# Kernel tuning notes

Measured on AMD Instinct MI355X. Metric: run time of the kernel, lower is better.

Reference implementation:

```python
import jax, jax.numpy as jnp
import numpy as np

B, S, D, H, L, O = 64, 512, 512, 1024, 2, 1000


def setup_inputs() -> dict:
    key = jax.random.key(0)
    ks = jax.random.split(key, 12)
    s = 0.05
    return {
        "x": jax.random.normal(ks[0], (B, S, D), jnp.float32),
        "h0": jnp.zeros((L, B, H), jnp.float32),
        "c0": jnp.zeros((L, B, H), jnp.float32),
        "W_ih0": jax.random.normal(ks[1], (4 * H, D), jnp.float32) * s,
        "W_hh0": jax.random.normal(ks[2], (4 * H, H), jnp.float32) * s,
        "b_ih0": jax.random.normal(ks[3], (4 * H,), jnp.float32) * s,
        "b_hh0": jax.random.normal(ks[4], (4 * H,), jnp.float32) * s,
        "W_ih1": jax.random.normal(ks[5], (4 * H, H), jnp.float32) * s,
        "W_hh1": jax.random.normal(ks[6], (4 * H, H), jnp.float32) * s,
        "b_ih1": jax.random.normal(ks[7], (4 * H,), jnp.float32) * s,
        "b_hh1": jax.random.normal(ks[8], (4 * H,), jnp.float32) * s,
        "W_fc": jax.random.normal(ks[9], (O, H), jnp.float32) * s,
        "b_fc": jax.random.normal(ks[10], (O,), jnp.float32) * s,
    }


def _lstm_cell(x_t, h, c, W_ih, W_hh, b_ih, b_hh):
    # standard LSTMCell: fused 4-gate GEMM, gate order (i, f, g, o)
    gates = x_t @ W_ih.T + b_ih + h @ W_hh.T + b_hh  # [B, 4H]
    i, f, g, o = jnp.split(gates, 4, axis=-1)
    i = jax.nn.sigmoid(i)
    f = jax.nn.sigmoid(f)
    g = jnp.tanh(g)
    o = jax.nn.sigmoid(o)
    c_new = f * c + i * g
    h_new = o * jnp.tanh(c_new)
    return h_new, c_new


def reference(x, h0, c0, W_ih0, W_hh0, b_ih0, b_hh0, W_ih1, W_hh1, b_ih1, b_hh1, W_fc, b_fc):
    params = [(W_ih0, W_hh0, b_ih0, b_hh0), (W_ih1, W_hh1, b_ih1, b_hh1)]

    def step(carry, x_t):
        hs, cs = carry  # tuples of [B,H] per layer
        new_h, new_c = [], []
        inp = x_t
        for l in range(L):  # fixed small layer count
            h_l, c_l = _lstm_cell(inp, hs[l], cs[l], *params[l])
            new_h.append(h_l)
            new_c.append(c_l)
            inp = h_l
        return (tuple(new_h), tuple(new_c)), None

    xs = jnp.swapaxes(x, 0, 1)  # [S, B, D]
    init = (tuple(h0[l] for l in range(L)), tuple(c0[l] for l in range(L)))
    (hs, _), _ = jax.lax.scan(step, init, xs)
    # dropout is inference-mode identity; output_activation=None
    out = hs[-1] @ W_fc.T + b_fc  # [B, O]
    return out
```

## Files before the change

### kernel.cpp

```cpp
#include <hip/hip_runtime.h>

#define B_ 64
#define S_ 512
#define D_ 512
#define H_ 1024

typedef __attribute__((ext_vector_type(8))) short bf16x8;
typedef __attribute__((ext_vector_type(4))) float f32x4;
typedef unsigned short u16;
typedef unsigned int u32;

#define MFMA(a, b, c) __builtin_amdgcn_mfma_f32_16x16x32_bf16(a, b, c, 0, 0, 0)

__device__ __forceinline__ u16 f2bf(float f) {
    u32 u = __float_as_uint(f);
    u += 0x7fffu + ((u >> 16) & 1u);
    return (u16)(u >> 16);
}
__device__ __forceinline__ float sigm(float x) { return 1.0f / (1.0f + __expf(-x)); }
__device__ __forceinline__ float tanh_f(float x) { return 1.0f - 2.0f / (__expf(2.0f * x) + 1.0f); }

__device__ __forceinline__ bf16x8 cvt8(const float* p) {
    float4 f0 = ((const float4*)p)[0];
    float4 f1 = ((const float4*)p)[1];
    bf16x8 v;
    v[0] = (short)f2bf(f0.x); v[1] = (short)f2bf(f0.y);
    v[2] = (short)f2bf(f0.z); v[3] = (short)f2bf(f0.w);
    v[4] = (short)f2bf(f1.x); v[5] = (short)f2bf(f1.y);
    v[6] = (short)f2bf(f1.z); v[7] = (short)f2bf(f1.w);
    return v;
}

__device__ __forceinline__ void llc_ld(bf16x8& d, const u16* p) {
    asm volatile("global_load_dwordx4 %0, %1, off sc0 sc1" : "=v"(d) : "v"(p));
}
__device__ __forceinline__ void vm0() {
    asm volatile("s_waitcnt vmcnt(0)" ::: "memory");
}
__device__ __forceinline__ void fence_frag(bf16x8& d) {
    asm volatile("" : "+v"(d));
}
__device__ __forceinline__ void llc_st16(u16* p, u16 v) {
    u32 vv = v;
    asm volatile("global_store_short %0, %1, off sc0 sc1" :: "v"(p), "v"(vv) : "memory");
}

__global__ void prep_w(const float* __restrict__ Wih, const float* __restrict__ Whh,
                       u16* __restrict__ Wc, int Kx, int Kw, int total8) {
    int idx = blockIdx.x * 256 + threadIdx.x;
    if (idx >= total8) return;
    int kc8 = Kw >> 3;
    int n = idx / kc8;
    int kc = (idx - n * kc8) << 3;
    const float* src = (kc < Kx) ? (Wih + (size_t)n * Kx + kc)
                                 : (Whh + (size_t)n * (Kw - Kx) + (kc - Kx));
    *(bf16x8*)(Wc + (size_t)n * Kw + kc) = cvt8(src);
}

__global__ void prep_misc2(const float* __restrict__ h0in,
                           const float* __restrict__ bih0, const float* __restrict__ bhh0,
                           const float* __restrict__ bih1, const float* __restrict__ bhh1,
                           float* __restrict__ bias0, float* __restrict__ bias1,
                           u16* __restrict__ h0a, u16* __restrict__ h0b,
                           u16* __restrict__ h1a, u16* __restrict__ h1b,
                           int* __restrict__ bar) {
    int idx = blockIdx.x * 256 + threadIdx.x;
    if (idx < 1024) bar[idx] = 0;
    if (idx < 4096) { bias0[idx] = bih0[idx] + bhh0[idx]; return; }
    if (idx < 8192) { int i = idx - 4096; bias1[i] = bih1[i] + bhh1[i]; return; }
    int r = idx - 8192;
    if (r >= 2 * B_ * H_) return;
    int l = r >> 16;
    int rr = r & 65535;
    int b = rr >> 10, col = rr & 1023;
    int sidx = (col >> 3) * 512 + b * 8 + (col & 7);
    u16 hb = f2bf(h0in[r]);
    if (l == 0) { h0a[sidx] = hb; h0b[sidx] = hb; }
    else        { h1a[sidx] = hb; h1b[sidx] = hb; }
}

__global__ __launch_bounds__(512, 2) void lstm_persist(
    const float* __restrict__ x,
    const u16* __restrict__ W0c, const u16* __restrict__ W1c,
    const float* __restrict__ bias0, const float* __restrict__ bias1,
    const float* __restrict__ c0in,
    u16* __restrict__ h0a, u16* __restrict__ h0b,
    u16* __restrict__ h1a, u16* __restrict__ h1b,
    float* __restrict__ h1f,
    int* __restrict__ bar) {
    const int bk = blockIdx.x;
    const int cgp = bk >> 1;
    const int mh = bk & 1;
    const int tid = threadIdx.x;
    const int w = tid >> 6;
    const int lane = tid & 63;
    const int quad = lane >> 4;
    const int l16 = lane & 15;

    int gc[2];
    #pragma unroll
    for (int n = 0; n < 2; ++n) {
        int c = n * 16 + l16;
        gc[n] = (c >> 3) * 1024 + cgp * 8 + (c & 7);
    }

    bf16x8 w0x[2][2], w0h[2][4];
    bf16x8 w1f[2][8];
    #pragma unroll
    for (int n = 0; n < 2; ++n) {
        #pragma unroll
        for (int kf = 0; kf < 2; ++kf)
            w0x[n][kf] = *(const bf16x8*)(W0c + (size_t)gc[n] * 1536 + w * 64 + kf * 32 + quad * 8);
        #pragma unroll
        for (int kf = 0; kf < 4; ++kf)
            w0h[n][kf] = *(const bf16x8*)(W0c + (size_t)gc[n] * 1536 + 512 + w * 128 + kf * 32 + quad * 8);
        #pragma unroll
        for (int kf = 0; kf < 8; ++kf)
            w1f[n][kf] = *(const bf16x8*)(W1c + (size_t)gc[n] * 2048 + w * 256 + kf * 32 + quad * 8);
    }

    __shared__ float part[8 * 32 * 37];
    __shared__ float c0l[256], c1l[256];
    __shared__ float b0l[32], b1l[32];

    if (tid < 32) {
        int gg = tid >> 3, j = tid & 7;
        b0l[tid] = bias0[gg * 1024 + cgp * 8 + j];
        b1l[tid] = bias1[gg * 1024 + cgp * 8 + j];
    }
    if (tid < 256) {
        int b = tid >> 3, j = tid & 7;
        int gi = (mh * 32 + b) * 1024 + cgp * 8 + j;
        c0l[tid] = c0in[gi];
        c1l[tid] = c0in[65536 + gi];
    }
    __syncthreads();

    const int brow0 = mh * 32 + l16;
    const int brow1 = brow0 + 16;

    f32x4 xacc[2][2];
    #define XPART(t)                                                                 \
        {                                                                            \
            xacc[0][0] = (f32x4){0.f,0.f,0.f,0.f}; xacc[0][1] = (f32x4){0.f,0.f,0.f,0.f}; \
            xacc[1][0] = (f32x4){0.f,0.f,0.f,0.f}; xacc[1][1] = (f32x4){0.f,0.f,0.f,0.f}; \
            _Pragma("unroll")                                                        \
            for (int kf = 0; kf < 2; ++kf) {                                         \
                int k = w * 64 + kf * 32 + quad * 8;                                 \
                bf16x8 a0_ = cvt8(x + (size_t)brow0 * 262144 + (t) * 512 + k);       \
                bf16x8 a1_ = cvt8(x + (size_t)brow1 * 262144 + (t) * 512 + k);       \
                xacc[0][0] = MFMA(a0_, w0x[0][kf], xacc[0][0]);                      \
                xacc[0][1] = MFMA(a0_, w0x[1][kf], xacc[0][1]);                      \
                xacc[1][0] = MFMA(a1_, w0x[0][kf], xacc[1][0]);                      \
                xacc[1][1] = MFMA(a1_, w0x[1][kf], xacc[1][1]);                      \
            }                                                                        \
        }

    XPART(0);

    for (int p = 0; p <= S_; ++p) {
        const int rd = p & 1;
        const u16* h0r = rd ? h0b : h0a;
        u16*       h0w_ = rd ? h0a : h0b;
        const u16* h1r = rd ? h1b : h1a;
        u16*       h1w_ = rd ? h1a : h1b;

        if (p > 0) {
            if (tid == 0) {
                int target = 256 * p;
                for (int it = 0; it < 20000; ++it) {
                    if (__hip_atomic_load(&bar[0], __ATOMIC_RELAXED, __HIP_MEMORY_SCOPE_AGENT) >= target)
                        break;
                    __builtin_amdgcn_s_sleep(1);
                }
            }
            __syncthreads();
        }

        bf16x8 a0[4], a1[4];
        if (p < S_) {
            #pragma unroll
            for (int kf = 0; kf < 4; ++kf) {
                int k8 = w * 16 + kf * 4 + quad;
                llc_ld(a0[kf], h0r + (k8 * 64 + brow0) * 8);
                llc_ld(a1[kf], h0r + (k8 * 64 + brow1) * 8);
            }
            vm0();
            #pragma unroll
            for (int kf = 0; kf < 4; ++kf) { fence_frag(a0[kf]); fence_frag(a1[kf]); }
        }
        bf16x8 pb0[8], pb1[8];
        if (p >= 1) {
            #pragma unroll
            for (int kf = 0; kf < 8; ++kf) {
                int k = w * 256 + kf * 32;
                const u16* src = (k < 1024) ? h0r : h1r;
                int k8 = ((k & 1023) >> 3) + quad;
                llc_ld(pb0[kf], src + (k8 * 64 + brow0) * 8);
                llc_ld(pb1[kf], src + (k8 * 64 + brow1) * 8);
            }
        }

        if (p < S_) {
            f32x4 acc00 = xacc[0][0], acc01 = xacc[0][1];
            f32x4 acc10 = xacc[1][0], acc11 = xacc[1][1];
            #pragma unroll
            for (int kf = 0; kf < 4; ++kf) {
                acc00 = MFMA(a0[kf], w0h[0][kf], acc00);
                acc01 = MFMA(a0[kf], w0h[1][kf], acc01);
                acc10 = MFMA(a1[kf], w0h[0][kf], acc10);
                acc11 = MFMA(a1[kf], w0h[1][kf], acc11);
            }
            #pragma unroll
            for (int r = 0; r < 4; ++r) {
                int r0 = quad * 4 + r, r1 = 16 + quad * 4 + r;
                part[w * 1184 + r0 * 37 + l16]      = acc00[r];
                part[w * 1184 + r0 * 37 + 16 + l16] = acc01[r];
                part[w * 1184 + r1 * 37 + l16]      = acc10[r];
                part[w * 1184 + r1 * 37 + 16 + l16] = acc11[r];
            }
            __syncthreads();
            if (tid < 256) {
                int b = tid >> 3, j = tid & 7;
                float g4[4];
                #pragma unroll
                for (int gg = 0; gg < 4; ++gg) {
                    float s = b0l[gg * 8 + j];
                    #pragma unroll
                    for (int w8 = 0; w8 < 8; ++w8)
                        s += part[w8 * 1184 + b * 37 + gg * 8 + j];
                    g4[gg] = s;
                }
                float c = c0l[tid];
                float cn = sigm(g4[1]) * c + sigm(g4[0]) * tanh_f(g4[2]);
                float hn = sigm(g4[3]) * tanh_f(cn);
                c0l[tid] = cn;
                llc_st16(h0w_ + cgp * 512 + (mh * 32 + b) * 8 + j, f2bf(hn));
            }
            __syncthreads();
        }

        if (p >= 1) {
            vm0();
            #pragma unroll
            for (int kf = 0; kf < 8; ++kf) { fence_frag(pb0[kf]); fence_frag(pb1[kf]); }
            f32x4 acc00 = {0.f,0.f,0.f,0.f}, acc01 = {0.f,0.f,0.f,0.f};
            f32x4 acc10 = {0.f,0.f,0.f,0.f}, acc11 = {0.f,0.f,0.f,0.f};
            #pragma unroll
            for (int kf = 0; kf < 8; ++kf) {
                acc00 = MFMA(pb0[kf], w1f[0][kf], acc00);
                acc01 = MFMA(pb0[kf], w1f[1][kf], acc01);
                acc10 = MFMA(pb1[kf], w1f[0][kf], acc10);
                acc11 = MFMA(pb1[kf], w1f[1][kf], acc11);
            }
            #pragma unroll
            for (int r = 0; r < 4; ++r) {
                int r0 = quad * 4 + r, r1 = 16 + quad * 4 + r;
                part[w * 1184 + r0 * 37 + l16]      = acc00[r];
                part[w * 1184 + r0 * 37 + 16 + l16] = acc01[r];
                part[w * 1184 + r1 * 37 + l16]      = acc10[r];
                part[w * 1184 + r1 * 37 + 16 + l16] = acc11[r];
            }
            __syncthreads();
            if (tid < 256) {
                int b = tid >> 3, j = tid & 7;
                float g4[4];
                #pragma unroll
                for (int gg = 0; gg < 4; ++gg) {
                    float s = b1l[gg * 8 + j];
                    #pragma unroll
                    for (int w8 = 0; w8 < 8; ++w8)
                        s += part[w8 * 1184 + b * 37 + gg * 8 + j];
                    g4[gg] = s;
                }
                float c = c1l[tid];
                float cn = sigm(g4[1]) * c + sigm(g4[0]) * tanh_f(g4[2]);
                float hn = sigm(g4[3]) * tanh_f(cn);
                c1l[tid] = cn;
                llc_st16(h1w_ + cgp * 512 + (mh * 32 + b) * 8 + j, f2bf(hn));
                if (p == S_) h1f[(mh * 32 + b) * 1024 + cgp * 8 + j] = hn;
            }
            __syncthreads();
        }

        if (p < S_) {
            if (tid == 0)
                __hip_atomic_fetch_add(&bar[0], 1, __ATOMIC_RELAXED, __HIP_MEMORY_SCOPE_AGENT);
            if (p + 1 < S_) XPART(p + 1);
        }
    }
}

__global__ void fc_k(const float* __restrict__ h1f, const float* __restrict__ Wfc,
                     const float* __restrict__ bfc, float* __restrict__ out) {
    int idx = blockIdx.x * 256 + threadIdx.x;
    if (idx >= 64 * 1000) return;
    int o = idx % 1000;
    int b = idx / 1000;
    const float4* hr = (const float4*)(h1f + b * H_);
    const float4* wr = (const float4*)(Wfc + (size_t)o * H_);
    float s = 0.f;
    #pragma unroll 4
    for (int k = 0; k < 256; ++k) {
        float4 a = hr[k];
        float4 w = wr[k];
        s += a.x * w.x + a.y * w.y + a.z * w.z + a.w * w.w;
    }
    out[idx] = s + bfc[o];
}

extern "C" void kernel_launch(void* const* d_in, const int* in_sizes, int n_in,
                              void* d_out, int out_size, void* d_ws, size_t ws_size,
                              hipStream_t stream) {
    const float* x    = (const float*)d_in[0];
    const float* h0in = (const float*)d_in[1];
    const float* c0in = (const float*)d_in[2];
    const float* Wih0 = (const float*)d_in[3];
    const float* Whh0 = (const float*)d_in[4];
    const float* bih0 = (const float*)d_in[5];
    const float* bhh0 = (const float*)d_in[6];
    const float* Wih1 = (const float*)d_in[7];
    const float* Whh1 = (const float*)d_in[8];
    const float* bih1 = (const float*)d_in[9];
    const float* bhh1 = (const float*)d_in[10];
    const float* Wfc  = (const float*)d_in[11];
    const float* bfc  = (const float*)d_in[12];
    float* out = (float*)d_out;

    char* ws = (char*)d_ws;
    size_t off = 0;
    auto alloc = [&](size_t bytes) {
        void* p = ws + off;
        off += (bytes + 255) & ~(size_t)255;
        return p;
    };
    u16* W0c   = (u16*)alloc((size_t)4096 * 1536 * 2);
    u16* W1c   = (u16*)alloc((size_t)4096 * 2048 * 2);
    float* bias0 = (float*)alloc(4096 * 4);
    float* bias1 = (float*)alloc(4096 * 4);
    u16* h0A   = (u16*)alloc(B_ * H_ * 2);
    u16* h0B   = (u16*)alloc(B_ * H_ * 2);
    u16* h1A   = (u16*)alloc(B_ * H_ * 2);
    u16* h1B   = (u16*)alloc(B_ * H_ * 2);
    float* h1f = (float*)alloc(B_ * H_ * 4);
    int* bar   = (int*)alloc(4096);

    prep_w<<<786432 / 256, 256, 0, stream>>>(Wih0, Whh0, W0c, 512, 1536, 786432);
    prep_w<<<1048576 / 256, 256, 0, stream>>>(Wih1, Whh1, W1c, 1024, 2048, 1048576);
    prep_misc2<<<(8192 + 2 * B_ * H_ + 255) / 256, 256, 0, stream>>>(
        h0in, bih0, bhh0, bih1, bhh1, bias0, bias1, h0A, h0B, h1A, h1B, bar);

    void* args[] = {(void*)&x, (void*)&W0c, (void*)&W1c, (void*)&bias0, (void*)&bias1,
                    (void*)&c0in, (void*)&h0A, (void*)&h0B, (void*)&h1A, (void*)&h1B,
                    (void*)&h1f, (void*)&bar};
    hipLaunchCooperativeKernel((void*)lstm_persist, dim3(256), dim3(512), args, 0, stream);

    fc_k<<<(64000 + 255) / 256, 256, 0, stream>>>(h1f, Wfc, bfc, out);
}
```

Measured before the change: 5.408 ms.

## Replace atomic counter grid barrier with per-block flags and broadcast epochs

Replaces the single shared atomic counter barrier with per-block padded flag stores. A master wave in block 0 gathers the flags and publishes the epoch to 32 replicated cache lines. Other blocks spin-poll their replica through LLC-coherent loads without sleeping. The aim is to remove atomic contention on one address and the sleep-induced wakeup delay in each timestep's grid sync. In exchange it adds a two-hop gather/broadcast latency and busy polling traffic.

Result: slower. 6.119 ms (+13.1%).

```diff
diff --git a/kernel.cpp b/kernel.cpp
--- a/kernel.cpp
+++ b/kernel.cpp
@@ -43,6 +43,26 @@
 __device__ __forceinline__ void llc_st16(u16* p, u16 v) {
     u32 vv = v;
     asm volatile("global_store_short %0, %1, off sc0 sc1" :: "v"(p), "v"(vv) : "memory");
+}
+__device__ __forceinline__ void llc_st32(int* p, int v) {
+    asm volatile("global_store_dword %0, %1, off sc0 sc1" :: "v"(p), "v"(v) : "memory");
+}
+__device__ __forceinline__ int llc_poll1(const int* p) {
+    int v;
+    asm volatile("global_load_dword %0, %1, off sc0 sc1\ns_waitcnt vmcnt(0)"
+                 : "=v"(v) : "v"(p) : "memory");
+    return v;
+}
+__device__ __forceinline__ void llc_ld_i4(int& v0, int& v1, int& v2, int& v3,
+                                          const int* p0, const int* p1,
+                                          const int* p2, const int* p3) {
+    asm volatile("global_load_dword %0, %4, off sc0 sc1\n"
+                 "global_load_dword %1, %5, off sc0 sc1\n"
+                 "global_load_dword %2, %6, off sc0 sc1\n"
+                 "global_load_dword %3, %7, off sc0 sc1\n"
+                 "s_waitcnt vmcnt(0)"
+                 : "=&v"(v0), "=&v"(v1), "=&v"(v2), "=&v"(v3)
+                 : "v"(p0), "v"(p1), "v"(p2), "v"(p3) : "memory");
 }
 
 __global__ void prep_w(const float* __restrict__ Wih, const float* __restrict__ Whh,
@@ -65,7 +85,7 @@
                            u16* __restrict__ h1a, u16* __restrict__ h1b,
                            int* __restrict__ bar) {
     int idx = blockIdx.x * 256 + threadIdx.x;
-    if (idx < 1024) bar[idx] = 0;
+    if (idx < 9216) bar[idx] = 0;
     if (idx < 4096) { bias0[idx] = bih0[idx] + bhh0[idx]; return; }
     if (idx < 8192) { int i = idx - 4096; bias1[i] = bih1[i] + bhh1[i]; return; }
     int r = idx - 8192;
@@ -167,11 +187,9 @@
 
         if (p > 0) {
             if (tid == 0) {
-                int target = 256 * p;
-                for (int it = 0; it < 20000; ++it) {
-                    if (__hip_atomic_load(&bar[0], __ATOMIC_RELAXED, __HIP_MEMORY_SCOPE_AGENT) >= target)
-                        break;
-                    __builtin_amdgcn_s_sleep(1);
+                const int* ep = bar + 8192 + (bk & 31) * 32;
+                for (int it = 0; it < 400000; ++it) {
+                    if (llc_poll1(ep) >= p) break;
                 }
             }
             __syncthreads();
@@ -284,8 +302,22 @@
         }
 
         if (p < S_) {
-            if (tid == 0)
-                __hip_atomic_fetch_add(&bar[0], 1, __ATOMIC_RELAXED, __HIP_MEMORY_SCOPE_AGENT);
+            if (tid == 0) llc_st32(bar + bk * 32, p + 1);
+            if (bk == 0 && w == 0) {
+                const int* f0 = bar + (lane * 4 + 0) * 32;
+                const int* f1 = bar + (lane * 4 + 1) * 32;
+                const int* f2 = bar + (lane * 4 + 2) * 32;
+                const int* f3 = bar + (lane * 4 + 3) * 32;
+                for (int it = 0; it < 200000; ++it) {
+                    int v0, v1, v2, v3;
+                    llc_ld_i4(v0, v1, v2, v3, f0, f1, f2, f3);
+                    int mn = v0 < v1 ? v0 : v1;
+                    int mn2 = v2 < v3 ? v2 : v3;
+                    mn = mn < mn2 ? mn : mn2;
+                    if (__all(mn >= p + 1)) break;
+                }
+                if (lane < 32) llc_st32(bar + 8192 + lane * 32, p + 1);
+            }
             if (p + 1 < S_) XPART(p + 1);
         }
     }
@@ -343,11 +375,11 @@
     u16* h1A   = (u16*)alloc(B_ * H_ * 2);
     u16* h1B   = (u16*)alloc(B_ * H_ * 2);
     float* h1f = (float*)alloc(B_ * H_ * 4);
-    int* bar   = (int*)alloc(4096);
+    int* bar   = (int*)alloc(40960);
 
     prep_w<<<786432 / 256, 256, 0, stream>>>(Wih0, Whh0, W0c, 512, 1536, 786432);
     prep_w<<<1048576 / 256, 256, 0, stream>>>(Wih1, Whh1, W1c, 1024, 2048, 1048576);
-    prep_misc2<<<(8192 + 2 * B_ * H_ + 255) / 256, 256, 0, stream>>>(
+    prep_misc2<<<(9216 + 2 * B_ * H_ + 255) / 256, 256, 0, stream>>>(
         h0in, bih0, bhh0, bih1, bhh1, bias0, bias1, h0A, h0B, h1A, h1B, bar);
 
     void* args[] = {(void*)&x, (void*)&W0c, (void*)&W1c, (void*)&bias0, (void*)&bias1,
```
